# Optimization experiments

Measured on AMD Instinct MI355X. Metric: run time of the kernel, lower is better.

## Reference

```python
import jax, jax.numpy as jnp
import numpy as np

B, N, D, L, NREPEAT = 32, 577, 384, 12, 4
H = 4 * D  # mlp hidden
EPS = 1e-6


def ln(x, w, b):
    mu = jnp.mean(x, axis=-1, keepdims=True)
    var = jnp.mean(jnp.square(x - mu), axis=-1, keepdims=True)
    return (x - mu) * jax.lax.rsqrt(var + EPS) * w + b


def setup_inputs() -> dict:
    key = jax.random.key(0)
    ks = jax.random.split(key, 16)
    s = 0.02
    return {
        "x": jax.random.normal(ks[0], (B, N, D), dtype=jnp.float32),
        "norm1_w": jnp.ones((L, D), jnp.float32),
        "norm1_b": jnp.zeros((L, D), jnp.float32),
        "qkv_w": jax.random.normal(ks[1], (L, 3 * D, D), jnp.float32) * s,
        "qkv_b": jnp.zeros((L, 3 * D), jnp.float32),
        "qn_w": jnp.ones((L, D), jnp.float32),
        "qn_b": jnp.zeros((L, D), jnp.float32),
        "kn_w": jnp.ones((L, D), jnp.float32),
        "kn_b": jnp.zeros((L, D), jnp.float32),
        "an_w": jnp.ones((L, D), jnp.float32),
        "an_b": jnp.zeros((L, D), jnp.float32),
        "proj_w": jax.random.normal(ks[2], (L, D, D), jnp.float32) * s,
        "proj_b": jnp.zeros((L, D), jnp.float32),
        "ls1": jnp.full((L, D), 1e-5, jnp.float32),
        "norm2_w": jnp.ones((L, D), jnp.float32),
        "norm2_b": jnp.zeros((L, D), jnp.float32),
        "fc1_w": jax.random.normal(ks[3], (L, H, D), jnp.float32) * s,
        "fc1_b": jnp.zeros((L, H), jnp.float32),
        "fc2_w": jax.random.normal(ks[4], (L, D, H), jnp.float32) * s,
        "fc2_b": jnp.zeros((L, D), jnp.float32),
        "ls2": jnp.full((L, D), 1e-5, jnp.float32),
    }


def _forward(x, norm1_w, norm1_b, qkv_w, qkv_b, qn_w, qn_b, kn_w, kn_b,
             an_w, an_b, proj_w, proj_b, ls1, norm2_w, norm2_b,
             fc1_w, fc1_b, fc2_w, fc2_b, ls2):
    scale = 1.0 / np.sqrt(D).astype(np.float32)
    x_prime = x
    history = []  # list of [B, 1, D] cls tokens, grows each repeat
    for _ in range(NREPEAT):
        new_cls = x[:, 0:1]
        x = jnp.concatenate([new_cls, x_prime[:, 1:]], axis=1)  # [B, N, D]
        mem = jnp.concatenate([x] + history, axis=1)            # [B, N+t, D]
        for l in range(L):
            res1 = x
            xn = ln(x, norm1_w[l], norm1_b[l])
            # manual qkv split: q from normed x, k/v from UNNORMED mem
            q = xn @ qkv_w[l, :D].T + qkv_b[l, :D]
            k = mem @ qkv_w[l, D:2 * D].T + qkv_b[l, D:2 * D]
            v = mem @ qkv_w[l, 2 * D:].T + qkv_b[l, 2 * D:]
            q = ln(q, qn_w[l], qn_b[l])
            k = ln(k, kn_w[l], kn_b[l])
            # single-head SDPA over full width D
            attn = jax.nn.softmax(jnp.einsum('bqd,bkd->bqk', q, k) * scale, axis=-1)
            prod = jnp.einsum('bqk,bkd->bqd', attn, v)
            prod = ln(prod, an_w[l], an_b[l])
            proj = prod @ proj_w[l].T + proj_b[l]
            x = proj * ls1[l] + res1
            res2 = x
            x2 = ln(x, norm2_w[l], norm2_b[l])
            h = jax.nn.gelu(x2 @ fc1_w[l].T + fc1_b[l], approximate=False)
            x1 = h @ fc2_w[l].T + fc2_b[l]
            x = x1 * ls2[l] + res2
        history.append(new_cls)
    return x


def reference(x, norm1_w, norm1_b, qkv_w, qkv_b, qn_w, qn_b, kn_w, kn_b,
              an_w, an_b, proj_w, proj_b, ls1, norm2_w, norm2_b,
              fc1_w, fc1_b, fc2_w, fc2_b, ls2):
    return _forward(x, norm1_w, norm1_b, qkv_w, qkv_b, qn_w, qn_b, kn_w, kn_b,
                    an_w, an_b, proj_w, proj_b, ls1, norm2_w, norm2_b,
                    fc1_w, fc1_b, fc2_w, fc2_b, ls2)
```

## Files before the change

### kernel.cpp

```cpp
#include <hip/hip_runtime.h>
#include <math.h>

#define BB 32
#define NN 577
#define DD 384
#define HD 1536
#define LL 12
#define MP 640
#define NRPT 4

typedef __attribute__((ext_vector_type(8))) short bf16x8;
typedef __attribute__((ext_vector_type(4))) float f32x4;

__device__ __forceinline__ unsigned short f2bf(float f){
  unsigned u = __builtin_bit_cast(unsigned, f);
  u += 0x7fffu + ((u >> 16) & 1u);
  return (unsigned short)(u >> 16);
}
__device__ __forceinline__ float bf2f(unsigned short s){
  unsigned u = ((unsigned)s) << 16;
  return __builtin_bit_cast(float, u);
}

__device__ __forceinline__ void async16(void* lds, const void* g){
  __builtin_amdgcn_global_load_lds(
      (const __attribute__((address_space(1))) unsigned int*)g,
      (__attribute__((address_space(3))) unsigned int*)lds, 16, 0, 0);
}

__global__ void prep_k(float* __restrict__ x, const float* __restrict__ xp,
                       float* __restrict__ cls_r, const float* __restrict__ cls_hist,
                       unsigned short* __restrict__ mem, int r){
  int i = blockIdx.x * 256 + threadIdx.x;
  if (i >= BB*MP*DD) return;
  int d = i % DD;
  int n = (i / DD) % MP;
  int b = i / (MP*DD);
  float v;
  if (n == 0){ v = x[(size_t)b*NN*DD + d]; cls_r[b*DD + d] = v; }
  else if (n < NN){ v = xp[((size_t)b*NN + n)*DD + d]; x[((size_t)b*NN + n)*DD + d] = v; }
  else if (n < NN + r){ v = cls_hist[(size_t)(n-NN)*BB*DD + b*DD + d]; }
  else v = 0.f;
  mem[i] = f2bf(v);
}

__global__ void cast_all_k(const float* __restrict__ qkvw, const float* __restrict__ pw,
                           const float* __restrict__ f1w, const float* __restrict__ f2w,
                           unsigned short* __restrict__ wbuf){
  int i = blockIdx.x * 256 + threadIdx.x;
  const int QKV = 3*DD*DD;
  const int PRJ = DD*DD;
  const int F1  = HD*DD;
  const int TOT = QKV + PRJ + 2*F1;
  if (i >= LL*TOT) return;
  int l = i / TOT, j = i % TOT;
  float v;
  if (j < QKV) v = qkvw[(size_t)l*QKV + j];
  else if (j < QKV+PRJ) v = pw[(size_t)l*PRJ + (j-QKV)];
  else if (j < QKV+PRJ+F1) v = f1w[(size_t)l*F1 + (j-QKV-PRJ)];
  else v = f2w[(size_t)l*F1 + (j-QKV-PRJ-F1)];
  wbuf[i] = f2bf(v);
}

template<typename T>
__global__ __launch_bounds__(256) void ln4_k(const T* __restrict__ in, const float* __restrict__ w,
                                             const float* __restrict__ bias, unsigned short* __restrict__ out,
                                             int nrows){
  int row = blockIdx.x*4 + (threadIdx.x >> 6);
  if (row >= nrows) return;
  int lane = threadIdx.x & 63;
  const T* p = in + (size_t)row*DD;
  float v[6];
  if constexpr (sizeof(T) == 4){
    const float* pf = (const float*)p;
    float4 a = *(const float4*)(pf + lane*4);
    float2 c = *(const float2*)(pf + 256 + lane*2);
    v[0]=a.x; v[1]=a.y; v[2]=a.z; v[3]=a.w; v[4]=c.x; v[5]=c.y;
  } else {
    const unsigned short* ps = (const unsigned short*)p;
    ushort4 a = *(const ushort4*)(ps + lane*4);
    ushort2 c = *(const ushort2*)(ps + 256 + lane*2);
    v[0]=bf2f(a.x); v[1]=bf2f(a.y); v[2]=bf2f(a.z); v[3]=bf2f(a.w);
    v[4]=bf2f(c.x); v[5]=bf2f(c.y);
  }
  float s = v[0]+v[1]+v[2]+v[3]+v[4]+v[5];
  #pragma unroll
  for (int o=32;o;o>>=1) s += __shfl_xor(s, o, 64);
  float mu = s * (1.f/DD);
  float q = 0.f;
  #pragma unroll
  for (int i=0;i<6;i++){ float t = v[i]-mu; q += t*t; }
  #pragma unroll
  for (int o=32;o;o>>=1) q += __shfl_xor(q, o, 64);
  float rs = rsqrtf(q*(1.f/DD) + 1e-6f);
  float4 w4 = *(const float4*)(w + lane*4);
  float2 w2 = *(const float2*)(w + 256 + lane*2);
  float4 b4 = *(const float4*)(bias + lane*4);
  float2 b2 = *(const float2*)(bias + 256 + lane*2);
  unsigned short* po = out + (size_t)row*DD;
  ushort4 o4;
  o4.x = f2bf((v[0]-mu)*rs*w4.x + b4.x);
  o4.y = f2bf((v[1]-mu)*rs*w4.y + b4.y);
  o4.z = f2bf((v[2]-mu)*rs*w4.z + b4.z);
  o4.w = f2bf((v[3]-mu)*rs*w4.w + b4.w);
  *(ushort4*)(po + lane*4) = o4;
  ushort2 o2;
  o2.x = f2bf((v[4]-mu)*rs*w2.x + b2.x);
  o2.y = f2bf((v[5]-mu)*rs*w2.y + b2.y);
  *(ushort2*)(po + 256 + lane*2) = o2;
}

template<int EPI>
__global__ __launch_bounds__(256) void gemm128(
    const unsigned short* __restrict__ A, int lda, int arows, long sA,
    const unsigned short* __restrict__ B, int ldb, int brows, long sB,
    const float* __restrict__ bias,
    int K, int N,
    float* __restrict__ outF, unsigned short* __restrict__ outB,
    int ldo, int orows, long sO,
    const float* __restrict__ ls){

  __shared__ unsigned short a_sh[2][128*32];
  __shared__ unsigned short b_sh[2][128*32];

  int tid  = threadIdx.x;
  int wave = tid >> 6, lane = tid & 63;
  int lr = lane & 15, kg = lane >> 4;
  int wm = wave >> 1, wn = wave & 1;
  int z = blockIdx.z;
  int row0 = blockIdx.y * 128;
  int col0 = blockIdx.x * 128;

  const unsigned short* Ab = A + (size_t)z*sA;
  const unsigned short* Bb = B + (size_t)z*sB;

  f32x4 zf = {0.f,0.f,0.f,0.f};
  f32x4 acc[4][4];
  #pragma unroll
  for (int i=0;i<4;i++)
    #pragma unroll
    for (int j=0;j<4;j++) acc[i][j] = zf;

  int ra[2], rb[2], kc[2];
  #pragma unroll
  for (int it=0; it<2; it++){
    int c = tid + it*256;
    int r = row0 + (c>>2); if (r > arows-1) r = arows-1;
    ra[it] = r;
    r = col0 + (c>>2); if (r > brows-1) r = brows-1;
    rb[it] = r;
    kc[it] = (c&3)*8;
  }

  for (int k0 = 0; k0 < K; k0 += 64){
    #pragma unroll
    for (int p=0;p<2;p++){
      #pragma unroll
      for (int it=0; it<2; it++){
        unsigned short* la = &a_sh[p][(it*256 + wave*64)*8];
        unsigned short* lb = &b_sh[p][(it*256 + wave*64)*8];
        async16(la, Ab + (size_t)ra[it]*lda + k0 + p*32 + kc[it]);
        async16(lb, Bb + (size_t)rb[it]*ldb + k0 + p*32 + kc[it]);
      }
    }
    __syncthreads();
    #pragma unroll
    for (int p=0;p<2;p++){
      bf16x8 af[4], bfr[4];
      #pragma unroll
      for (int i=0;i<4;i++){
        af[i]  = *(const bf16x8*)&a_sh[p][(wm*64 + i*16 + lr)*32 + kg*8];
        bfr[i] = *(const bf16x8*)&b_sh[p][(wn*64 + i*16 + lr)*32 + kg*8];
      }
      #pragma unroll
      for (int i=0;i<4;i++)
        #pragma unroll
        for (int j=0;j<4;j++)
          acc[i][j] = __builtin_amdgcn_mfma_f32_16x16x32_bf16(af[i], bfr[j], acc[i][j], 0,0,0);
    }
    __syncthreads();
  }

  float* oF = outF ? outF + (size_t)z*sO : nullptr;
  unsigned short* oB = outB ? outB + (size_t)z*sO : nullptr;

  #pragma unroll
  for (int mi=0;mi<4;mi++)
    #pragma unroll
    for (int ni=0;ni<4;ni++)
      #pragma unroll
      for (int r=0;r<4;r++){
        int row = row0 + wm*64 + mi*16 + kg*4 + r;
        int col = col0 + wn*64 + ni*16 + lr;
        if (row >= orows || col >= N) continue;
        float vv = acc[mi][ni][r];
        size_t idx = (size_t)row*ldo + col;
        if (EPI == 0){
          if (bias) vv += bias[col];
          oB[idx] = f2bf(vv);
        } else if (EPI == 1){
          vv += bias[row];
          oB[idx] = f2bf(vv);
        } else if (EPI == 2){
          vv += bias[col];
          oF[idx] = vv*ls[col] + oF[idx];
        } else {
          vv += bias[col];
          float g = 0.5f*vv*(1.f + erff(vv*0.70710678118f));
          oB[idx] = f2bf(g);
        }
      }
}

__global__ __launch_bounds__(256, 2) void attn_k(
    const unsigned short* __restrict__ qraw,
    const float* __restrict__ qw, const float* __restrict__ qb_,
    const unsigned short* __restrict__ kb,
    const unsigned short* __restrict__ vT,
    const float* __restrict__ anw, const float* __restrict__ anb,
    unsigned short* __restrict__ out, int M){

  __shared__ unsigned short k_sh[32*384];
  __shared__ unsigned short v_sh[384*32];
  __shared__ unsigned short p_sh[64*56];

  int tid = threadIdx.x;
  int wv = tid >> 6, lane = tid & 63;
  int lr = lane & 15, kg = lane >> 4;
  int b = blockIdx.y, qt0 = blockIdx.x * 64;

  bf16x8 qf[12];
  {
    int qrow = qt0 + wv*16 + lr; if (qrow > NN-1) qrow = NN-1;
    const unsigned short* qp = qraw + ((size_t)b*NN + qrow)*DD;
    float s1 = 0.f, s2 = 0.f;
    #pragma unroll
    for (int ks=0; ks<12; ks++){
      qf[ks] = *(const bf16x8*)(qp + ks*32 + kg*8);
      #pragma unroll
      for (int j=0;j<8;j++){
        float t = bf2f((unsigned short)qf[ks][j]);
        s1 += t; s2 += t*t;
      }
    }
    s1 += __shfl_xor(s1, 16, 64); s1 += __shfl_xor(s1, 32, 64);
    s2 += __shfl_xor(s2, 16, 64); s2 += __shfl_xor(s2, 32, 64);
    const float SC = 0.05103103588f;
    float mu = s1 * (1.f/DD);
    float var = s2 * (1.f/DD) - mu*mu;
    float rs = rsqrtf(fmaxf(var, 0.f) + 1e-6f) * SC;
    #pragma unroll
    for (int ks=0; ks<12; ks++){
      int c0 = ks*32 + kg*8;
      float4 wa = *(const float4*)(qw + c0);
      float4 wb = *(const float4*)(qw + c0 + 4);
      float4 ba = *(const float4*)(qb_ + c0);
      float4 bb = *(const float4*)(qb_ + c0 + 4);
      bf16x8 t;
      t[0] = (short)f2bf((bf2f((unsigned short)qf[ks][0])-mu)*rs*wa.x + ba.x*SC);
      t[1] = (short)f2bf((bf2f((unsigned short)qf[ks][1])-mu)*rs*wa.y + ba.y*SC);
      t[2] = (short)f2bf((bf2f((unsigned short)qf[ks][2])-mu)*rs*wa.z + ba.z*SC);
      t[3] = (short)f2bf((bf2f((unsigned short)qf[ks][3])-mu)*rs*wa.w + ba.w*SC);
      t[4] = (short)f2bf((bf2f((unsigned short)qf[ks][4])-mu)*rs*wb.x + bb.x*SC);
      t[5] = (short)f2bf((bf2f((unsigned short)qf[ks][5])-mu)*rs*wb.y + bb.y*SC);
      t[6] = (short)f2bf((bf2f((unsigned short)qf[ks][6])-mu)*rs*wb.z + bb.z*SC);
      t[7] = (short)f2bf((bf2f((unsigned short)qf[ks][7])-mu)*rs*wb.w + bb.w*SC);
      qf[ks] = t;
    }
  }

  f32x4 zf = {0.f,0.f,0.f,0.f};
  f32x4 O[24];
  #pragma unroll
  for (int i=0;i<24;i++) O[i] = zf;
  float m_run[4], l_run[4];
  #pragma unroll
  for (int r=0;r<4;r++){ m_run[r] = -INFINITY; l_run[r] = 0.f; }

  for (int kt=0; kt<19; kt++){
    __syncthreads();
    #pragma unroll
    for (int i=0;i<6;i++){
      int L = i*256 + tid;
      int row = L/48, c = L%48;
      int gc = (c & ~7) | ((c ^ row) & 7);
      async16(&k_sh[L*8], kb + ((size_t)b*MP + kt*32 + row)*DD + gc*8);
    }
    #pragma unroll
    for (int i=0;i<6;i++){
      int L = i*256 + tid;
      int row = L>>2;
      int gc = (L&3) ^ (row&3);
      async16(&v_sh[L*8], vT + ((size_t)b*DD + row)*MP + kt*32 + gc*8);
    }
    __syncthreads();

    f32x4 s[2] = {zf, zf};
    __builtin_amdgcn_s_setprio(1);
    #pragma unroll
    for (int ks=0; ks<12; ks++){
      int c = ks*4 + kg;
      #pragma unroll
      for (int nk=0; nk<2; nk++){
        int krow = nk*16 + lr;
        bf16x8 bk = *(const bf16x8*)&k_sh[krow*DD + ((c & ~7) | ((c ^ krow)&7))*8];
        s[nk] = __builtin_amdgcn_mfma_f32_16x16x32_bf16(qf[ks], bk, s[nk], 0,0,0);
      }
    }
    __builtin_amdgcn_s_setprio(0);
    #pragma unroll
    for (int nk=0; nk<2; nk++){
      if (kt*32 + nk*16 + lr >= M){
        s[nk][0] = -INFINITY; s[nk][1] = -INFINITY; s[nk][2] = -INFINITY; s[nk][3] = -INFINITY;
      }
    }
    float vmax[4];
    #pragma unroll
    for (int r=0;r<4;r++){
      float v = fmaxf(s[0][r], s[1][r]);
      v = fmaxf(v, __shfl_xor(v, 1, 64));
      v = fmaxf(v, __shfl_xor(v, 2, 64));
      v = fmaxf(v, __shfl_xor(v, 4, 64));
      v = fmaxf(v, __shfl_xor(v, 8, 64));
      vmax[r] = v;
    }
    bool small = (vmax[0] <= m_run[0] + 8.f) & (vmax[1] <= m_run[1] + 8.f)
               & (vmax[2] <= m_run[2] + 8.f) & (vmax[3] <= m_run[3] + 8.f);
    if (!__all(small)){
      #pragma unroll
      for (int r=0;r<4;r++){
        float mn = fmaxf(m_run[r], vmax[r]);
        float al = __expf(m_run[r] - mn);
        m_run[r] = mn;
        l_run[r] *= al;
        #pragma unroll
        for (int ni=0;ni<24;ni++) O[ni][r] *= al;
      }
    }
    #pragma unroll
    for (int nk=0;nk<2;nk++)
      #pragma unroll
      for (int r=0;r<4;r++)
        s[nk][r] = __expf(s[nk][r] - m_run[r]);
    #pragma unroll
    for (int r=0;r<4;r++){
      float v = s[0][r] + s[1][r];
      v += __shfl_xor(v, 1, 64);
      v += __shfl_xor(v, 2, 64);
      v += __shfl_xor(v, 4, 64);
      v += __shfl_xor(v, 8, 64);
      l_run[r] += v;
    }
    #pragma unroll
    for (int nk=0;nk<2;nk++)
      #pragma unroll
      for (int r=0;r<4;r++)
        p_sh[(wv*16 + kg*4 + r)*56 + nk*16 + lr] = f2bf(s[nk][r]);
    __syncthreads();

    bf16x8 ap = *(const bf16x8*)&p_sh[(wv*16 + lr)*56 + kg*8];
    __builtin_amdgcn_s_setprio(1);
    #pragma unroll
    for (int ni=0;ni<24;ni++){
      int d = ni*16 + lr;
      bf16x8 bv = *(const bf16x8*)&v_sh[d*32 + ((kg ^ (d&3))*8)];
      O[ni] = __builtin_amdgcn_mfma_f32_16x16x32_bf16(ap, bv, O[ni], 0,0,0);
    }
    __builtin_amdgcn_s_setprio(0);
  }

  float inv[4];
  #pragma unroll
  for (int r=0;r<4;r++) inv[r] = 1.f / l_run[r];
  float s1[4] = {0,0,0,0}, s2[4] = {0,0,0,0};
  #pragma unroll
  for (int ni=0;ni<24;ni++)
    #pragma unroll
    for (int r=0;r<4;r++){
      float x = O[ni][r]*inv[r];
      O[ni][r] = x;
      s1[r] += x; s2[r] += x*x;
    }
  #pragma unroll
  for (int r=0;r<4;r++){
    #pragma unroll
    for (int o=1;o<16;o<<=1){ s1[r] += __shfl_xor(s1[r], o, 64); s2[r] += __shfl_xor(s2[r], o, 64); }
  }
  float mu[4], rs[4];
  #pragma unroll
  for (int r=0;r<4;r++){
    mu[r] = s1[r]*(1.f/DD);
    float var = s2[r]*(1.f/DD) - mu[r]*mu[r];
    rs[r] = rsqrtf(fmaxf(var, 0.f) + 1e-6f);
  }
  int rowb = qt0 + wv*16 + kg*4;
  #pragma unroll
  for (int ni=0;ni<24;ni++){
    int col = ni*16 + lr;
    float wc = anw[col], bc = anb[col];
    #pragma unroll
    for (int r=0;r<4;r++){
      int qrow = rowb + r;
      if (qrow < NN)
        out[((size_t)b*NN + qrow)*DD + col] = f2bf((O[ni][r]-mu[r])*rs[r]*wc + bc);
    }
  }
}


extern "C" void kernel_launch(void* const* d_in, const int* in_sizes, int n_in,
                              void* d_out, int out_size, void* d_ws, size_t ws_size,
                              hipStream_t stream){
  const float* x_in = (const float*)d_in[0];
  const float* n1w  = (const float*)d_in[1];
  const float* n1b  = (const float*)d_in[2];
  const float* qkvw = (const float*)d_in[3];
  const float* qkvb = (const float*)d_in[4];
  const float* qnw  = (const float*)d_in[5];
  const float* qnb  = (const float*)d_in[6];
  const float* knw  = (const float*)d_in[7];
  const float* knb  = (const float*)d_in[8];
  const float* anw  = (const float*)d_in[9];
  const float* anb  = (const float*)d_in[10];
  const float* pw   = (const float*)d_in[11];
  const float* pb   = (const float*)d_in[12];
  const float* ls1  = (const float*)d_in[13];
  const float* n2w  = (const float*)d_in[14];
  const float* n2b  = (const float*)d_in[15];
  const float* f1w  = (const float*)d_in[16];
  const float* f1b  = (const float*)d_in[17];
  const float* f2w  = (const float*)d_in[18];
  const float* f2bb = (const float*)d_in[19];
  const float* ls2  = (const float*)d_in[20];

  char* ws = (char*)d_ws;
  size_t off = 0;
  auto alloc = [&](size_t bytes)->char* {
    char* p = ws + off;
    off = (off + bytes + 255) & ~(size_t)255;
    return p;
  };

  const int QKV = 3*DD*DD, PRJ = DD*DD, F1 = HD*DD;
  const size_t WTOT = (size_t)QKV + PRJ + 2*F1;
  const size_t SLOT = (size_t)BB*MP*DD;

  unsigned short* wbuf  = (unsigned short*)alloc((size_t)LL*WTOT*2);
  float*          cls_h = (float*)         alloc((size_t)NRPT*BB*DD*4);
  unsigned short* mem_bf= (unsigned short*)alloc(SLOT*2);
  unsigned short* pool  = (unsigned short*)alloc(6*SLOT*2);

  unsigned short* S0 = pool;
  unsigned short* S1 = pool + SLOT;
  unsigned short* S2 = pool + 2*SLOT;
  unsigned short* S3 = pool + 3*SLOT;
  unsigned short* S5 = pool + 5*SLOT;

  unsigned short* xn    = S0;
  unsigned short* qraw  = S1;
  unsigned short* kraw  = S2;
  unsigned short* vT    = S5;
  unsigned short* prodn = S3;
  unsigned short* x2    = S0;
  unsigned short* h     = S1;

  float* xf = (float*)d_out;

  auto cg = [](size_t n){ return dim3((unsigned)((n + 255) / 256)); };

  hipMemcpyAsync(xf, x_in, (size_t)BB*NN*DD*4, hipMemcpyDeviceToDevice, stream);

  const int RT  = (BB*NN + 127)/128;
  const int RTM = (BB*MP)/128;
  const int QR  = BB*NN;
  const int KR  = BB*MP;

  cast_all_k<<<cg((size_t)LL*WTOT),256,0,stream>>>(qkvw, pw, f1w, f2w, wbuf);

  for (int r = 0; r < NRPT; r++){
    int M = NN + r;
    prep_k<<<cg((size_t)BB*MP*DD),256,0,stream>>>(xf, x_in, cls_h + (size_t)r*BB*DD, cls_h, mem_bf, r);
    for (int l = 0; l < LL; l++){
      const unsigned short* wl = wbuf + (size_t)l*WTOT;
      const unsigned short* wq = wl;
      const unsigned short* wp = wl + QKV;
      const unsigned short* w1 = wl + QKV + PRJ;
      const unsigned short* w2 = wl + QKV + PRJ + F1;

      ln4_k<float><<<cg((size_t)QR*64),256,0,stream>>>(xf, n1w + l*DD, n1b + l*DD, xn, QR);
      gemm128<0><<<dim3(3,RT,1),256,0,stream>>>(xn,384,QR,0, wq,384,384,0,
          qkvb + l*3*DD, 384,384, nullptr,qraw,384,QR,0, nullptr);
      gemm128<0><<<dim3(3,RTM,1),256,0,stream>>>(mem_bf,384,KR,0, wq + (size_t)DD*DD,384,384,0,
          qkvb + l*3*DD + DD, 384,384, nullptr,kraw,384,KR,0, nullptr);
      gemm128<1><<<dim3(MP/128,3,BB),256,0,stream>>>(wq + (size_t)2*DD*DD,384,384,0, mem_bf,384,MP,(long)MP*DD,
          qkvb + l*3*DD + 2*DD, 384,MP, nullptr,vT,MP,384,(long)DD*MP, nullptr);
      ln4_k<unsigned short><<<cg((size_t)KR*64),256,0,stream>>>(kraw, knw + l*DD, knb + l*DD, kraw, KR);
      attn_k<<<dim3(10,BB),256,0,stream>>>(qraw, qnw + l*DD, qnb + l*DD, kraw, vT,
                                           anw + l*DD, anb + l*DD, prodn, M);
      gemm128<2><<<dim3(3,RT,1),256,0,stream>>>(prodn,384,QR,0, wp,384,384,0,
          pb + l*DD, 384,384, xf,nullptr,384,QR,0, ls1 + l*DD);
      ln4_k<float><<<cg((size_t)QR*64),256,0,stream>>>(xf, n2w + l*DD, n2b + l*DD, x2, QR);
      gemm128<3><<<dim3(HD/128,RT,1),256,0,stream>>>(x2,384,QR,0, w1,384,HD,0,
          f1b + l*HD, 384,HD, nullptr,h,HD,QR,0, nullptr);
      gemm128<2><<<dim3(3,RT,1),256,0,stream>>>(h,HD,QR,0, w2,HD,384,0,
          f2bb + l*DD, HD,384, xf,nullptr,384,QR,0, ls2 + l*DD);
    }
  }
}
```

Before: 16.66 ms.

## Fuse LayerNorms into GEMM epilogues with full-row tiles and double-buffered K loop

Adds full-width (64x384) GEMM kernels that compute bias, residual, layer-scale and the following LayerNorm in the epilogue: Q/K projections now include q/k norm (and the attention scale), and the proj/fc2 GEMMs update the residual and emit norm2/next-layer norm1 outputs. This removes the standalone LN kernels and their extra activation round trips, and merges the Q and K GEMMs into one launch. The generic GEMM loop also switches to a 32-wide double-buffered prefetch with one barrier per step. Full-row tiles lower the block count and may reduce occupancy. The one-pass variance may be less accurate.

```diff
diff --git a/kernel.cpp b/kernel.cpp
--- a/kernel.cpp
+++ b/kernel.cpp
@@ -71,18 +71,10 @@
   int lane = threadIdx.x & 63;
   const T* p = in + (size_t)row*DD;
   float v[6];
-  if constexpr (sizeof(T) == 4){
-    const float* pf = (const float*)p;
-    float4 a = *(const float4*)(pf + lane*4);
-    float2 c = *(const float2*)(pf + 256 + lane*2);
-    v[0]=a.x; v[1]=a.y; v[2]=a.z; v[3]=a.w; v[4]=c.x; v[5]=c.y;
-  } else {
-    const unsigned short* ps = (const unsigned short*)p;
-    ushort4 a = *(const ushort4*)(ps + lane*4);
-    ushort2 c = *(const ushort2*)(ps + 256 + lane*2);
-    v[0]=bf2f(a.x); v[1]=bf2f(a.y); v[2]=bf2f(a.z); v[3]=bf2f(a.w);
-    v[4]=bf2f(c.x); v[5]=bf2f(c.y);
-  }
+  const float* pf = (const float*)p;
+  float4 a = *(const float4*)(pf + lane*4);
+  float2 c = *(const float2*)(pf + 256 + lane*2);
+  v[0]=a.x; v[1]=a.y; v[2]=a.z; v[3]=a.w; v[4]=c.x; v[5]=c.y;
   float s = v[0]+v[1]+v[2]+v[3]+v[4]+v[5];
   #pragma unroll
   for (int o=32;o;o>>=1) s += __shfl_xor(s, o, 64);
@@ -152,32 +144,34 @@
     kc[it] = (c&3)*8;
   }
 
-  for (int k0 = 0; k0 < K; k0 += 64){
-    #pragma unroll
-    for (int p=0;p<2;p++){
-      #pragma unroll
-      for (int it=0; it<2; it++){
-        unsigned short* la = &a_sh[p][(it*256 + wave*64)*8];
-        unsigned short* lb = &b_sh[p][(it*256 + wave*64)*8];
-        async16(la, Ab + (size_t)ra[it]*lda + k0 + p*32 + kc[it]);
-        async16(lb, Bb + (size_t)rb[it]*ldb + k0 + p*32 + kc[it]);
-      }
-    }
-    __syncthreads();
-    #pragma unroll
-    for (int p=0;p<2;p++){
-      bf16x8 af[4], bfr[4];
-      #pragma unroll
-      for (int i=0;i<4;i++){
-        af[i]  = *(const bf16x8*)&a_sh[p][(wm*64 + i*16 + lr)*32 + kg*8];
-        bfr[i] = *(const bf16x8*)&b_sh[p][(wn*64 + i*16 + lr)*32 + kg*8];
-      }
-      #pragma unroll
-      for (int i=0;i<4;i++)
-        #pragma unroll
-        for (int j=0;j<4;j++)
-          acc[i][j] = __builtin_amdgcn_mfma_f32_16x16x32_bf16(af[i], bfr[j], acc[i][j], 0,0,0);
-    }
+  auto stage = [&](int buf, int k){
+    #pragma unroll
+    for (int it=0; it<2; it++){
+      unsigned short* la = &a_sh[buf][(it*256 + wave*64)*8];
+      unsigned short* lb = &b_sh[buf][(it*256 + wave*64)*8];
+      async16(la, Ab + (size_t)ra[it]*lda + k + kc[it]);
+      async16(lb, Bb + (size_t)rb[it]*ldb + k + kc[it]);
+    }
+  };
+
+  int nt = K >> 5;
+  stage(0, 0);
+  __syncthreads();
+  #pragma unroll 2
+  for (int t=0; t<nt; t++){
+    int cur = t & 1;
+    if (t+1 < nt) stage(cur^1, (t+1)*32);
+    bf16x8 af[4], bfr[4];
+    #pragma unroll
+    for (int i=0;i<4;i++){
+      af[i]  = *(const bf16x8*)&a_sh[cur][(wm*64 + i*16 + lr)*32 + kg*8];
+      bfr[i] = *(const bf16x8*)&b_sh[cur][(wn*64 + i*16 + lr)*32 + kg*8];
+    }
+    #pragma unroll
+    for (int i=0;i<4;i++)
+      #pragma unroll
+      for (int j=0;j<4;j++)
+        acc[i][j] = __builtin_amdgcn_mfma_f32_16x16x32_bf16(af[i], bfr[j], acc[i][j], 0,0,0);
     __syncthreads();
   }
 
@@ -212,9 +206,258 @@
       }
 }
 
+__global__ __launch_bounds__(256, 2) void gemmqk(
+    const unsigned short* __restrict__ Aq, int qrows, int qtiles,
+    const unsigned short* __restrict__ Ak, int krows,
+    const unsigned short* __restrict__ W,
+    const float* __restrict__ bias,
+    const float* __restrict__ qnw, const float* __restrict__ qnb,
+    const float* __restrict__ knw, const float* __restrict__ knb,
+    unsigned short* __restrict__ qout, unsigned short* __restrict__ kout){
+
+  __shared__ unsigned short a_sh[2][64*32];
+  __shared__ unsigned short b_sh[2][384*32];
+  __shared__ float red_sh[2][4][64];
+
+  int tid = threadIdx.x;
+  int wv = tid >> 6, lane = tid & 63;
+  int lr = lane & 15, kg = lane >> 4;
+
+  bool isq = blockIdx.x < qtiles;
+  int row0 = (isq ? blockIdx.x : blockIdx.x - qtiles) * 64;
+  const unsigned short* A = isq ? Aq : Ak;
+  int arows = isq ? qrows : krows;
+  const unsigned short* Wb = isq ? W : W + (size_t)DD*DD;
+  const float* bcol = isq ? bias : bias + DD;
+  const float* lw = isq ? qnw : knw;
+  const float* lb = isq ? qnb : knb;
+  unsigned short* out = isq ? qout : kout;
+  float scale = isq ? 0.05103103588f : 1.0f;
+
+  int arow = row0 + (tid>>2); if (arow > arows-1) arow = arows-1;
+  int akoff = (tid&3)*8;
+
+  f32x4 zf = {0,0,0,0};
+  f32x4 acc[4][6];
+  #pragma unroll
+  for (int i=0;i<4;i++)
+    #pragma unroll
+    for (int j=0;j<6;j++) acc[i][j] = zf;
+
+  auto stage = [&](int buf, int k){
+    async16(&a_sh[buf][(size_t)tid*8], A + (size_t)arow*DD + k + akoff);
+    #pragma unroll
+    for (int i=0;i<6;i++){
+      int c = i*256 + tid;
+      async16(&b_sh[buf][(size_t)c*8], Wb + (size_t)(c>>2)*DD + k + (c&3)*8);
+    }
+  };
+
+  stage(0, 0);
+  __syncthreads();
+  #pragma unroll 2
+  for (int t=0; t<12; t++){
+    int cur = t & 1;
+    if (t < 11) stage(cur^1, (t+1)*32);
+    bf16x8 af[4], bfr[6];
+    #pragma unroll
+    for (int mi=0;mi<4;mi++) af[mi] = *(const bf16x8*)&a_sh[cur][(mi*16 + lr)*32 + kg*8];
+    #pragma unroll
+    for (int ni=0;ni<6;ni++) bfr[ni] = *(const bf16x8*)&b_sh[cur][(wv*96 + ni*16 + lr)*32 + kg*8];
+    #pragma unroll
+    for (int mi=0;mi<4;mi++)
+      #pragma unroll
+      for (int ni=0;ni<6;ni++)
+        acc[mi][ni] = __builtin_amdgcn_mfma_f32_16x16x32_bf16(af[mi], bfr[ni], acc[mi][ni], 0,0,0);
+    __syncthreads();
+  }
+
+  float s1[4][4], s2[4][4];
+  #pragma unroll
+  for (int mi=0;mi<4;mi++)
+    #pragma unroll
+    for (int r=0;r<4;r++){ s1[mi][r]=0.f; s2[mi][r]=0.f; }
+  #pragma unroll
+  for (int ni=0;ni<6;ni++){
+    float bv = bcol[wv*96 + ni*16 + lr];
+    #pragma unroll
+    for (int mi=0;mi<4;mi++)
+      #pragma unroll
+      for (int r=0;r<4;r++){
+        float v = acc[mi][ni][r] + bv;
+        acc[mi][ni][r] = v;
+        s1[mi][r] += v; s2[mi][r] += v*v;
+      }
+  }
+  #pragma unroll
+  for (int mi=0;mi<4;mi++)
+    #pragma unroll
+    for (int r=0;r<4;r++){
+      #pragma unroll
+      for (int o=1;o<16;o<<=1){
+        s1[mi][r] += __shfl_xor(s1[mi][r], o, 64);
+        s2[mi][r] += __shfl_xor(s2[mi][r], o, 64);
+      }
+    }
+  if (lr == 0){
+    #pragma unroll
+    for (int mi=0;mi<4;mi++)
+      #pragma unroll
+      for (int r=0;r<4;r++){
+        red_sh[0][wv][mi*16 + kg*4 + r] = s1[mi][r];
+        red_sh[1][wv][mi*16 + kg*4 + r] = s2[mi][r];
+      }
+  }
+  __syncthreads();
+  #pragma unroll
+  for (int mi=0;mi<4;mi++){
+    #pragma unroll
+    for (int r=0;r<4;r++){
+      int rl = mi*16 + kg*4 + r;
+      float t1 = red_sh[0][0][rl] + red_sh[0][1][rl] + red_sh[0][2][rl] + red_sh[0][3][rl];
+      float t2 = red_sh[1][0][rl] + red_sh[1][1][rl] + red_sh[1][2][rl] + red_sh[1][3][rl];
+      float mu = t1*(1.f/DD);
+      float var = t2*(1.f/DD) - mu*mu;
+      float rs = rsqrtf(fmaxf(var, 0.f) + 1e-6f);
+      int grow = row0 + rl;
+      if (grow < arows){
+        #pragma unroll
+        for (int ni=0;ni<6;ni++){
+          int col = wv*96 + ni*16 + lr;
+          out[(size_t)grow*DD + col] = f2bf(((acc[mi][ni][r]-mu)*rs*lw[col] + lb[col])*scale);
+        }
+      }
+    }
+  }
+}
+
+__global__ __launch_bounds__(256, 2) void gemmln(
+    const unsigned short* __restrict__ A, int arows, int K,
+    const unsigned short* __restrict__ W,
+    const float* __restrict__ bias, const float* __restrict__ ls,
+    float* __restrict__ xf,
+    const float* __restrict__ lnw, const float* __restrict__ lnb,
+    unsigned short* __restrict__ outB){
+
+  __shared__ unsigned short a_sh[2][64*32];
+  __shared__ unsigned short b_sh[2][384*32];
+  __shared__ float red_sh[2][4][64];
+
+  int tid = threadIdx.x;
+  int wv = tid >> 6, lane = tid & 63;
+  int lr = lane & 15, kg = lane >> 4;
+  int row0 = blockIdx.x * 64;
+
+  int arow = row0 + (tid>>2); if (arow > arows-1) arow = arows-1;
+  int akoff = (tid&3)*8;
+
+  f32x4 zf = {0,0,0,0};
+  f32x4 acc[4][6];
+  #pragma unroll
+  for (int i=0;i<4;i++)
+    #pragma unroll
+    for (int j=0;j<6;j++) acc[i][j] = zf;
+
+  auto stage = [&](int buf, int k){
+    async16(&a_sh[buf][(size_t)tid*8], A + (size_t)arow*K + k + akoff);
+    #pragma unroll
+    for (int i=0;i<6;i++){
+      int c = i*256 + tid;
+      async16(&b_sh[buf][(size_t)c*8], W + (size_t)(c>>2)*K + k + (c&3)*8);
+    }
+  };
+
+  int nt = K >> 5;
+  stage(0, 0);
+  __syncthreads();
+  #pragma unroll 2
+  for (int t=0; t<nt; t++){
+    int cur = t & 1;
+    if (t+1 < nt) stage(cur^1, (t+1)*32);
+    bf16x8 af[4], bfr[6];
+    #pragma unroll
+    for (int mi=0;mi<4;mi++) af[mi] = *(const bf16x8*)&a_sh[cur][(mi*16 + lr)*32 + kg*8];
+    #pragma unroll
+    for (int ni=0;ni<6;ni++) bfr[ni] = *(const bf16x8*)&b_sh[cur][(wv*96 + ni*16 + lr)*32 + kg*8];
+    #pragma unroll
+    for (int mi=0;mi<4;mi++)
+      #pragma unroll
+      for (int ni=0;ni<6;ni++)
+        acc[mi][ni] = __builtin_amdgcn_mfma_f32_16x16x32_bf16(af[mi], bfr[ni], acc[mi][ni], 0,0,0);
+    __syncthreads();
+  }
+
+  float s1[4][4], s2[4][4];
+  #pragma unroll
+  for (int mi=0;mi<4;mi++)
+    #pragma unroll
+    for (int r=0;r<4;r++){ s1[mi][r]=0.f; s2[mi][r]=0.f; }
+  #pragma unroll
+  for (int ni=0;ni<6;ni++){
+    int col = wv*96 + ni*16 + lr;
+    float bv = bias[col];
+    float lv = ls[col];
+    #pragma unroll
+    for (int mi=0;mi<4;mi++)
+      #pragma unroll
+      for (int r=0;r<4;r++){
+        int grow = row0 + mi*16 + kg*4 + r;
+        float v = acc[mi][ni][r] + bv;
+        if (grow < arows){
+          size_t idx = (size_t)grow*DD + col;
+          v = v*lv + xf[idx];
+          xf[idx] = v;
+        }
+        acc[mi][ni][r] = v;
+        s1[mi][r] += v; s2[mi][r] += v*v;
+      }
+  }
+  if (outB){
+    #pragma unroll
+    for (int mi=0;mi<4;mi++)
+      #pragma unroll
+      for (int r=0;r<4;r++){
+        #pragma unroll
+        for (int o=1;o<16;o<<=1){
+          s1[mi][r] += __shfl_xor(s1[mi][r], o, 64);
+          s2[mi][r] += __shfl_xor(s2[mi][r], o, 64);
+        }
+      }
+    if (lr == 0){
+      #pragma unroll
+      for (int mi=0;mi<4;mi++)
+        #pragma unroll
+        for (int r=0;r<4;r++){
+          red_sh[0][wv][mi*16 + kg*4 + r] = s1[mi][r];
+          red_sh[1][wv][mi*16 + kg*4 + r] = s2[mi][r];
+        }
+    }
+    __syncthreads();
+    #pragma unroll
+    for (int mi=0;mi<4;mi++){
+      #pragma unroll
+      for (int r=0;r<4;r++){
+        int rl = mi*16 + kg*4 + r;
+        float t1 = red_sh[0][0][rl] + red_sh[0][1][rl] + red_sh[0][2][rl] + red_sh[0][3][rl];
+        float t2 = red_sh[1][0][rl] + red_sh[1][1][rl] + red_sh[1][2][rl] + red_sh[1][3][rl];
+        float mu = t1*(1.f/DD);
+        float var = t2*(1.f/DD) - mu*mu;
+        float rs = rsqrtf(fmaxf(var, 0.f) + 1e-6f);
+        int grow = row0 + rl;
+        if (grow < arows){
+          #pragma unroll
+          for (int ni=0;ni<6;ni++){
+            int col = wv*96 + ni*16 + lr;
+            outB[(size_t)grow*DD + col] = f2bf((acc[mi][ni][r]-mu)*rs*lnw[col] + lnb[col]);
+          }
+        }
+      }
+    }
+  }
+}
+
 __global__ __launch_bounds__(256, 2) void attn_k(
-    const unsigned short* __restrict__ qraw,
-    const float* __restrict__ qw, const float* __restrict__ qb_,
+    const unsigned short* __restrict__ qs,
     const unsigned short* __restrict__ kb,
     const unsigned short* __restrict__ vT,
     const float* __restrict__ anw, const float* __restrict__ anb,
@@ -232,41 +475,9 @@
   bf16x8 qf[12];
   {
     int qrow = qt0 + wv*16 + lr; if (qrow > NN-1) qrow = NN-1;
-    const unsigned short* qp = qraw + ((size_t)b*NN + qrow)*DD;
-    float s1 = 0.f, s2 = 0.f;
-    #pragma unroll
-    for (int ks=0; ks<12; ks++){
-      qf[ks] = *(const bf16x8*)(qp + ks*32 + kg*8);
-      #pragma unroll
-      for (int j=0;j<8;j++){
-        float t = bf2f((unsigned short)qf[ks][j]);
-        s1 += t; s2 += t*t;
-      }
-    }
-    s1 += __shfl_xor(s1, 16, 64); s1 += __shfl_xor(s1, 32, 64);
-    s2 += __shfl_xor(s2, 16, 64); s2 += __shfl_xor(s2, 32, 64);
-    const float SC = 0.05103103588f;
-    float mu = s1 * (1.f/DD);
-    float var = s2 * (1.f/DD) - mu*mu;
-    float rs = rsqrtf(fmaxf(var, 0.f) + 1e-6f) * SC;
-    #pragma unroll
-    for (int ks=0; ks<12; ks++){
-      int c0 = ks*32 + kg*8;
-      float4 wa = *(const float4*)(qw + c0);
-      float4 wb = *(const float4*)(qw + c0 + 4);
-      float4 ba = *(const float4*)(qb_ + c0);
-      float4 bb = *(const float4*)(qb_ + c0 + 4);
-      bf16x8 t;
-      t[0] = (short)f2bf((bf2f((unsigned short)qf[ks][0])-mu)*rs*wa.x + ba.x*SC);
-      t[1] = (short)f2bf((bf2f((unsigned short)qf[ks][1])-mu)*rs*wa.y + ba.y*SC);
-      t[2] = (short)f2bf((bf2f((unsigned short)qf[ks][2])-mu)*rs*wa.z + ba.z*SC);
-      t[3] = (short)f2bf((bf2f((unsigned short)qf[ks][3])-mu)*rs*wa.w + ba.w*SC);
-      t[4] = (short)f2bf((bf2f((unsigned short)qf[ks][4])-mu)*rs*wb.x + bb.x*SC);
-      t[5] = (short)f2bf((bf2f((unsigned short)qf[ks][5])-mu)*rs*wb.y + bb.y*SC);
-      t[6] = (short)f2bf((bf2f((unsigned short)qf[ks][6])-mu)*rs*wb.z + bb.z*SC);
-      t[7] = (short)f2bf((bf2f((unsigned short)qf[ks][7])-mu)*rs*wb.w + bb.w*SC);
-      qf[ks] = t;
-    }
+    const unsigned short* qp = qs + ((size_t)b*NN + qrow)*DD;
+    #pragma unroll
+    for (int ks=0; ks<12; ks++) qf[ks] = *(const bf16x8*)(qp + ks*32 + kg*8);
   }
 
   f32x4 zf = {0.f,0.f,0.f,0.f};
@@ -457,8 +668,8 @@
   unsigned short* S5 = pool + 5*SLOT;
 
   unsigned short* xn    = S0;
-  unsigned short* qraw  = S1;
-  unsigned short* kraw  = S2;
+  unsigned short* qb    = S1;
+  unsigned short* kb    = S2;
   unsigned short* vT    = S5;
   unsigned short* prodn = S3;
   unsigned short* x2    = S0;
@@ -471,9 +682,10 @@
   hipMemcpyAsync(xf, x_in, (size_t)BB*NN*DD*4, hipMemcpyDeviceToDevice, stream);
 
   const int RT  = (BB*NN + 127)/128;
-  const int RTM = (BB*MP)/128;
   const int QR  = BB*NN;
   const int KR  = BB*MP;
+  const int RTq = (QR + 63)/64;
+  const int RTk = KR/64;
 
   cast_all_k<<<cg((size_t)LL*WTOT),256,0,stream>>>(qkvw, pw, f1w, f2w, wbuf);
 
@@ -487,23 +699,22 @@
       const unsigned short* w1 = wl + QKV + PRJ;
       const unsigned short* w2 = wl + QKV + PRJ + F1;
 
-      ln4_k<float><<<cg((size_t)QR*64),256,0,stream>>>(xf, n1w + l*DD, n1b + l*DD, xn, QR);
-      gemm128<0><<<dim3(3,RT,1),256,0,stream>>>(xn,384,QR,0, wq,384,384,0,
-          qkvb + l*3*DD, 384,384, nullptr,qraw,384,QR,0, nullptr);
-      gemm128<0><<<dim3(3,RTM,1),256,0,stream>>>(mem_bf,384,KR,0, wq + (size_t)DD*DD,384,384,0,
-          qkvb + l*3*DD + DD, 384,384, nullptr,kraw,384,KR,0, nullptr);
+      if (l == 0)
+        ln4_k<float><<<cg((size_t)QR*64),256,0,stream>>>(xf, n1w, n1b, xn, QR);
+
+      gemmqk<<<dim3(RTq + RTk),256,0,stream>>>(xn, QR, RTq, mem_bf, KR, wq,
+          qkvb + l*3*DD, qnw + l*DD, qnb + l*DD, knw + l*DD, knb + l*DD, qb, kb);
       gemm128<1><<<dim3(MP/128,3,BB),256,0,stream>>>(wq + (size_t)2*DD*DD,384,384,0, mem_bf,384,MP,(long)MP*DD,
           qkvb + l*3*DD + 2*DD, 384,MP, nullptr,vT,MP,384,(long)DD*MP, nullptr);
-      ln4_k<unsigned short><<<cg((size_t)KR*64),256,0,stream>>>(kraw, knw + l*DD, knb + l*DD, kraw, KR);
-      attn_k<<<dim3(10,BB),256,0,stream>>>(qraw, qnw + l*DD, qnb + l*DD, kraw, vT,
-                                           anw + l*DD, anb + l*DD, prodn, M);
-      gemm128<2><<<dim3(3,RT,1),256,0,stream>>>(prodn,384,QR,0, wp,384,384,0,
-          pb + l*DD, 384,384, xf,nullptr,384,QR,0, ls1 + l*DD);
-      ln4_k<float><<<cg((size_t)QR*64),256,0,stream>>>(xf, n2w + l*DD, n2b + l*DD, x2, QR);
+      attn_k<<<dim3(10,BB),256,0,stream>>>(qb, kb, vT, anw + l*DD, anb + l*DD, prodn, M);
+      gemmln<<<dim3(RTq),256,0,stream>>>(prodn, QR, 384, wp, pb + l*DD, ls1 + l*DD,
+          xf, n2w + l*DD, n2b + l*DD, x2);
       gemm128<3><<<dim3(HD/128,RT,1),256,0,stream>>>(x2,384,QR,0, w1,384,HD,0,
           f1b + l*HD, 384,HD, nullptr,h,HD,QR,0, nullptr);
-      gemm128<2><<<dim3(3,RT,1),256,0,stream>>>(h,HD,QR,0, w2,HD,384,0,
-          f2bb + l*DD, HD,384, xf,nullptr,384,QR,0, ls2 + l*DD);
-    }
-  }
-}
+      gemmln<<<dim3(RTq),256,0,stream>>>(h, QR, 1536, w2, f2bb + l*DD, ls2 + l*DD,
+          xf, (l < LL-1) ? n1w + (l+1)*DD : nullptr,
+              (l < LL-1) ? n1b + (l+1)*DD : nullptr,
+              (l < LL-1) ? xn : nullptr);
+    }
+  }
+}
```

Result: no change. 16.94 ms (+1.7%).

## Cache per-layer K/V across repeats and recompute only the changed memory rows

Applied to the files above, without the earlier changes.

K and V are projected from the unnormalised memory sequence, and between repeats that sequence changes only in row 0 (the new cls token) and in the newly appended history row. On repeat 0 the full K/V (with K layernorm) is stored per layer in a workspace cache. Later repeats skip the K and V GEMMs and the K layernorm, and instead run a small fixup kernel that recomputes just those two rows for K (normalised) and V (transposed). This needs about 24 extra SLOT-sized buffers of workspace and falls back to the old path when ws_size is too small.

```diff
diff --git a/kernel.cpp b/kernel.cpp
--- a/kernel.cpp
+++ b/kernel.cpp
@@ -108,6 +108,64 @@
   o2.x = f2bf((v[4]-mu)*rs*w2.x + b2.x);
   o2.y = f2bf((v[5]-mu)*rs*w2.y + b2.y);
   *(ushort2*)(po + 256 + lane*2) = o2;
+}
+
+__global__ __launch_bounds__(256) void fixup_k(
+    const unsigned short* __restrict__ mem,
+    const unsigned short* __restrict__ wq,
+    const float* __restrict__ qkvb,
+    const float* __restrict__ knw, const float* __restrict__ knb,
+    unsigned short* __restrict__ kc,
+    unsigned short* __restrict__ vc,
+    int row2){
+  int task = blockIdx.x*4 + (threadIdx.x >> 6);
+  int lane = threadIdx.x & 63;
+  int kind = task & 1;
+  int rsel = (task >> 1) & 1;
+  int b    = task >> 2;
+  int row  = rsel ? row2 : 0;
+  const unsigned short* mrow = mem + ((size_t)b*MP + row)*DD;
+  const unsigned short* W = wq + (size_t)(kind+1)*DD*DD;
+  const float* bias = qkvb + (kind+1)*DD;
+
+  float acc[6] = {0,0,0,0,0,0};
+  for (int i=0;i<48;i++){
+    bf16x8 m8 = *(const bf16x8*)(mrow + i*8);
+    float mf[8];
+    #pragma unroll
+    for (int j=0;j<8;j++) mf[j] = bf2f((unsigned short)m8[j]);
+    #pragma unroll
+    for (int c=0;c<6;c++){
+      bf16x8 w8 = *(const bf16x8*)(W + (size_t)(lane + c*64)*DD + i*8);
+      #pragma unroll
+      for (int j=0;j<8;j++) acc[c] += mf[j]*bf2f((unsigned short)w8[j]);
+    }
+  }
+  #pragma unroll
+  for (int c=0;c<6;c++) acc[c] += bias[lane + c*64];
+
+  if (kind == 0){
+    float s1 = 0.f, s2 = 0.f;
+    #pragma unroll
+    for (int c=0;c<6;c++){ s1 += acc[c]; s2 += acc[c]*acc[c]; }
+    #pragma unroll
+    for (int o=32;o;o>>=1){ s1 += __shfl_xor(s1, o, 64); s2 += __shfl_xor(s2, o, 64); }
+    float mu = s1*(1.f/DD);
+    float var = s2*(1.f/DD) - mu*mu;
+    float rs = rsqrtf(fmaxf(var, 0.f) + 1e-6f);
+    unsigned short* out = kc + ((size_t)b*MP + row)*DD;
+    #pragma unroll
+    for (int c=0;c<6;c++){
+      int col = lane + c*64;
+      out[col] = f2bf((acc[c]-mu)*rs*knw[col] + knb[col]);
+    }
+  } else {
+    #pragma unroll
+    for (int c=0;c<6;c++){
+      int d = lane + c*64;
+      vc[((size_t)b*DD + d)*MP + row] = f2bf(acc[c]);
+    }
+  }
 }
 
 template<int EPI>
@@ -449,6 +507,9 @@
   float*          cls_h = (float*)         alloc((size_t)NRPT*BB*DD*4);
   unsigned short* mem_bf= (unsigned short*)alloc(SLOT*2);
   unsigned short* pool  = (unsigned short*)alloc(6*SLOT*2);
+  unsigned short* kcache = (unsigned short*)alloc((size_t)LL*SLOT*2);
+  unsigned short* vcache = (unsigned short*)alloc((size_t)LL*SLOT*2);
+  bool use_cache = (off <= ws_size);
 
   unsigned short* S0 = pool;
   unsigned short* S1 = pool + SLOT;
@@ -458,8 +519,6 @@
 
   unsigned short* xn    = S0;
   unsigned short* qraw  = S1;
-  unsigned short* kraw  = S2;
-  unsigned short* vT    = S5;
   unsigned short* prodn = S3;
   unsigned short* x2    = S0;
   unsigned short* h     = S1;
@@ -487,15 +546,25 @@
       const unsigned short* w1 = wl + QKV + PRJ;
       const unsigned short* w2 = wl + QKV + PRJ + F1;
 
+      unsigned short* kbuf = use_cache ? kcache + (size_t)l*SLOT : S2;
+      unsigned short* vbuf = use_cache ? vcache + (size_t)l*SLOT : S5;
+
       ln4_k<float><<<cg((size_t)QR*64),256,0,stream>>>(xf, n1w + l*DD, n1b + l*DD, xn, QR);
       gemm128<0><<<dim3(3,RT,1),256,0,stream>>>(xn,384,QR,0, wq,384,384,0,
           qkvb + l*3*DD, 384,384, nullptr,qraw,384,QR,0, nullptr);
-      gemm128<0><<<dim3(3,RTM,1),256,0,stream>>>(mem_bf,384,KR,0, wq + (size_t)DD*DD,384,384,0,
-          qkvb + l*3*DD + DD, 384,384, nullptr,kraw,384,KR,0, nullptr);
-      gemm128<1><<<dim3(MP/128,3,BB),256,0,stream>>>(wq + (size_t)2*DD*DD,384,384,0, mem_bf,384,MP,(long)MP*DD,
-          qkvb + l*3*DD + 2*DD, 384,MP, nullptr,vT,MP,384,(long)DD*MP, nullptr);
-      ln4_k<unsigned short><<<cg((size_t)KR*64),256,0,stream>>>(kraw, knw + l*DD, knb + l*DD, kraw, KR);
-      attn_k<<<dim3(10,BB),256,0,stream>>>(qraw, qnw + l*DD, qnb + l*DD, kraw, vT,
+
+      if (!use_cache || r == 0){
+        gemm128<0><<<dim3(3,RTM,1),256,0,stream>>>(mem_bf,384,KR,0, wq + (size_t)DD*DD,384,384,0,
+            qkvb + l*3*DD + DD, 384,384, nullptr,kbuf,384,KR,0, nullptr);
+        gemm128<1><<<dim3(MP/128,3,BB),256,0,stream>>>(wq + (size_t)2*DD*DD,384,384,0, mem_bf,384,MP,(long)MP*DD,
+            qkvb + l*3*DD + 2*DD, 384,MP, nullptr,vbuf,MP,384,(long)DD*MP, nullptr);
+        ln4_k<unsigned short><<<cg((size_t)KR*64),256,0,stream>>>(kbuf, knw + l*DD, knb + l*DD, kbuf, KR);
+      } else {
+        fixup_k<<<32,256,0,stream>>>(mem_bf, wq, qkvb + l*3*DD,
+                                     knw + l*DD, knb + l*DD, kbuf, vbuf, NN + r - 1);
+      }
+
+      attn_k<<<dim3(10,BB),256,0,stream>>>(qraw, qnw + l*DD, qnb + l*DD, kbuf, vbuf,
                                            anw + l*DD, anb + l*DD, prodn, M);
       gemm128<2><<<dim3(3,RT,1),256,0,stream>>>(prodn,384,QR,0, wp,384,384,0,
           pb + l*DD, 384,384, xf,nullptr,384,QR,0, ls1 + l*DD);
```

Measured after the change: 16.55 ms. Within noise of the previous version (-0.7%).
